# Optimization experiments

Measured on AMD Instinct MI355X. Metric: run time of the kernel, lower is better.

## Reference

```python
import math
import jax, jax.numpy as jnp
import numpy as np

B, T, C, H = 2, 4096, 512, 8  # batch, seq_len, n_embd, n_head
D = C // H                    # head_dim = 64

def setup_inputs() -> dict:
    key = jax.random.key(0)
    k1, k2, k3 = jax.random.split(key, 3)
    x = jax.random.normal(k1, (B, T, C), dtype=jnp.float32)
    # torch Linear(C, 3C, bias=False): y = x @ W.T; we store the transposed
    # weight directly so the forward is x @ W_attn.
    W_attn = jax.random.normal(k2, (C, 3 * C), dtype=jnp.float32) * 0.02
    W_proj = jax.random.normal(k3, (C, C), dtype=jnp.float32) * 0.02
    return {"x": x, "W_attn": W_attn, "W_proj": W_proj}

def reference(x, W_attn, W_proj):
    b, t, c = x.shape
    # fused QKV projection, split like .split(n_embd, dim=2)
    qkv = x @ W_attn                              # [B,T,3C]
    q, k, v = jnp.split(qkv, 3, axis=-1)          # each [B,T,C]
    def to_heads(u):
        return u.reshape(b, t, H, D).transpose(0, 2, 1, 3)  # [B,H,T,D]
    q, k, v = to_heads(q), to_heads(k), to_heads(v)
    scale = 1.0 / math.sqrt(D)
    att = jnp.einsum('bhqd,bhkd->bhqk', q, k) * scale       # [B,H,T,T]
    causal = jnp.tril(jnp.ones((t, t), dtype=bool))         # masked_fill(triu(...,1), -inf)
    att = jnp.where(causal, att, -jnp.inf)
    probs = jax.nn.softmax(att, axis=-1)
    y = jnp.einsum('bhqk,bhkd->bhqd', probs, v)             # [B,H,T,D]
    y = y.transpose(0, 2, 1, 3).reshape(b, t, c)            # [B,T,C]
    return y @ W_proj
```

## Files before the change

kernel.cpp:

```cpp
#include <hip/hip_runtime.h>
#include <hip/hip_bf16.h>
#include <stdint.h>


typedef __attribute__((ext_vector_type(8))) short short8;
typedef __attribute__((ext_vector_type(4))) float floatx4;

__device__ __forceinline__ unsigned short f2bf(float f) {
    unsigned int x = __float_as_uint(f);
    unsigned int r = x + 0x7fffu + ((x >> 16) & 1u);
    return (unsigned short)(r >> 16);
}

__device__ __forceinline__ unsigned int pk_bf16(float a, float b) {
    __hip_bfloat162 p = __float22bfloat162_rn(make_float2(a, b));
    return *reinterpret_cast<unsigned int*>(&p);
}

__global__ __launch_bounds__(256) void prep_a(
    const float* __restrict__ x, unsigned short* __restrict__ xb,
    const float* __restrict__ Wa, unsigned short* __restrict__ WaT)
{
    const int bid = blockIdx.x;
    const int tid = threadIdx.x;
    if (bid < 2048) {
        size_t i = ((size_t)bid * 256 + tid) * 8;
        float4 a = *reinterpret_cast<const float4*>(x + i);
        float4 b = *reinterpret_cast<const float4*>(x + i + 4);
        unsigned short o[8] = {f2bf(a.x), f2bf(a.y), f2bf(a.z), f2bf(a.w),
                               f2bf(b.x), f2bf(b.y), f2bf(b.z), f2bf(b.w)};
        *reinterpret_cast<uint4*>(xb + i) = *reinterpret_cast<uint4*>(o);
    } else {
        __shared__ unsigned short tile[32][34];
        const int t2 = bid - 2048;
        const int n0 = (t2 % 48) * 32, k0 = (t2 / 48) * 32;
        const int tx = tid & 31, ty = tid >> 5;
        #pragma unroll
        for (int p = 0; p < 4; ++p)
            tile[tx][ty + p * 8] = f2bf(Wa[(size_t)(k0 + ty + p * 8) * 1536 + n0 + tx]);
        __syncthreads();
        #pragma unroll
        for (int p = 0; p < 4; ++p)
            WaT[(size_t)(n0 + ty + p * 8) * 512 + k0 + tx] = tile[ty + p * 8][tx];
    }
}

__global__ __launch_bounds__(256) void transpose_wp(
    const float* __restrict__ W, unsigned short* __restrict__ Wt)
{
    __shared__ unsigned short tile[32][34];
    const int tid = threadIdx.x;
    const int tx = tid & 31, ty = tid >> 5;
    const int n0 = blockIdx.x * 32, k0 = blockIdx.y * 32;
    #pragma unroll
    for (int p = 0; p < 4; ++p)
        tile[tx][ty + p * 8] = f2bf(W[(size_t)(k0 + ty + p * 8) * 512 + n0 + tx]);
    __syncthreads();
    #pragma unroll
    for (int p = 0; p < 4; ++p)
        Wt[(size_t)(n0 + ty + p * 8) * 512 + k0 + tx] = tile[ty + p * 8][tx];
}

template<int EPI>
__global__ __launch_bounds__(256) void mm_bt(
    const unsigned short* __restrict__ A,
    const unsigned short* __restrict__ Bt,
    void* __restrict__ outp)
{
    __shared__ __align__(16) unsigned char smem[40960];

    const int tid  = threadIdx.x;
    const int wave = tid >> 6;
    const int lane = tid & 63;
    const int quad = lane >> 4;
    const int l16  = lane & 15;
    const int wr   = wave >> 1;
    const int wc   = wave & 1;
    const int m0 = blockIdx.x * 128;
    const int n0 = blockIdx.y * 128;

    floatx4 acc[4][4];
    #pragma unroll
    for (int i = 0; i < 4; ++i)
        #pragma unroll
        for (int j = 0; j < 4; ++j) acc[i][j] = (floatx4){0.f, 0.f, 0.f, 0.f};

    const int row = tid >> 1;
    const int cb  = (tid & 1) * 16;

    const unsigned short* ap = &A[(size_t)(m0 + row) * 512 + cb];
    const unsigned short* bp = &Bt[(size_t)(n0 + row) * 512 + cb];

    uint4 ra0 = *reinterpret_cast<const uint4*>(ap);
    uint4 ra1 = *reinterpret_cast<const uint4*>(ap + 8);
    uint4 rb0 = *reinterpret_cast<const uint4*>(bp);
    uint4 rb1 = *reinterpret_cast<const uint4*>(bp + 8);
    {
        auto Al = reinterpret_cast<unsigned short(*)[40]>(smem);
        auto Bl = reinterpret_cast<unsigned short(*)[40]>(smem + 10240);
        *reinterpret_cast<uint4*>(&Al[row][cb])     = ra0;
        *reinterpret_cast<uint4*>(&Al[row][cb + 8]) = ra1;
        *reinterpret_cast<uint4*>(&Bl[row][cb])     = rb0;
        *reinterpret_cast<uint4*>(&Bl[row][cb + 8]) = rb1;
    }

    for (int it = 0; it < 16; ++it) {
        __syncthreads();
        const int k0 = it * 32;
        if (it < 15) {
            ra0 = *reinterpret_cast<const uint4*>(ap + k0 + 32);
            ra1 = *reinterpret_cast<const uint4*>(ap + k0 + 40);
            rb0 = *reinterpret_cast<const uint4*>(bp + k0 + 32);
            rb1 = *reinterpret_cast<const uint4*>(bp + k0 + 40);
        }

        auto Al = reinterpret_cast<unsigned short(*)[40]>(smem + (it & 1) * 20480);
        auto Bl = reinterpret_cast<unsigned short(*)[40]>(smem + (it & 1) * 20480 + 10240);

        short8 af[4], bf[4];
        #pragma unroll
        for (int ti = 0; ti < 4; ++ti)
            af[ti] = *reinterpret_cast<const short8*>(&Al[wr * 64 + ti * 16 + l16][quad * 8]);
        #pragma unroll
        for (int tj = 0; tj < 4; ++tj)
            bf[tj] = *reinterpret_cast<const short8*>(&Bl[wc * 64 + tj * 16 + l16][quad * 8]);
        #pragma unroll
        for (int ti = 0; ti < 4; ++ti)
            #pragma unroll
            for (int tj = 0; tj < 4; ++tj)
                acc[ti][tj] = __builtin_amdgcn_mfma_f32_16x16x32_bf16(af[ti], bf[tj], acc[ti][tj], 0, 0, 0);

        if (it < 15) {
            auto An = reinterpret_cast<unsigned short(*)[40]>(smem + ((it + 1) & 1) * 20480);
            auto Bn = reinterpret_cast<unsigned short(*)[40]>(smem + ((it + 1) & 1) * 20480 + 10240);
            *reinterpret_cast<uint4*>(&An[row][cb])     = ra0;
            *reinterpret_cast<uint4*>(&An[row][cb + 8]) = ra1;
            *reinterpret_cast<uint4*>(&Bn[row][cb])     = rb0;
            *reinterpret_cast<uint4*>(&Bn[row][cb + 8]) = rb1;
        }
    }

    if (EPI == 0) {
        unsigned short* WS = (unsigned short*)outp;
        unsigned short* Qb  = WS;
        unsigned short* Kb  = WS + 4194304;
        unsigned short* Vtb = WS + 8388608;
        const int which = n0 >> 9;
        const int h = ((n0 + wc * 64) >> 6) & 7;

        if (which == 2) {
            auto Tr = reinterpret_cast<unsigned short(*)[80]>(smem);
            __syncthreads();
            #pragma unroll
            for (int ti = 0; ti < 4; ++ti)
                #pragma unroll
                for (int tj = 0; tj < 4; ++tj) {
                    unsigned int lo = pk_bf16(acc[ti][tj][0], acc[ti][tj][1]);
                    unsigned int hi = pk_bf16(acc[ti][tj][2], acc[ti][tj][3]);
                    *reinterpret_cast<uint2*>(&Tr[(wave << 6) + tj * 16 + l16][ti * 16 + quad * 4])
                        = make_uint2(lo, hi);
                }
            const int b = m0 >> 12;
            const int bh = b * 8 + h;
            const int t0g = (m0 & 4095) + wr * 64;
            const int tseg = (lane & 7) * 8;
            #pragma unroll
            for (int p = 0; p < 8; ++p) {
                int dl = p * 8 + (lane >> 3);
                uint4 v = *reinterpret_cast<const uint4*>(&Tr[(wave << 6) + dl][tseg]);
                *reinterpret_cast<uint4*>(&Vtb[((size_t)(bh * 64 + dl)) * 4096 + t0g + tseg]) = v;
            }
        } else {
            const float sc = (which == 0) ? 0.18033688f : 1.0f;
            #pragma unroll
            for (int ti = 0; ti < 4; ++ti) {
                #pragma unroll
                for (int r = 0; r < 4; ++r) {
                    int m = m0 + wr * 64 + ti * 16 + quad * 4 + r;
                    int b = m >> 12, t = m & 4095;
                    int bh = b * 8 + h;
                    #pragma unroll
                    for (int tj = 0; tj < 4; ++tj) {
                        int d = tj * 16 + l16;
                        unsigned short val = f2bf(acc[ti][tj][r] * sc);
                        if (which == 0) Qb[((size_t)bh * 4096 + t) * 64 + d] = val;
                        else            Kb[((size_t)bh * 4096 + t) * 64 + d] = val;
                    }
                }
            }
        }
    } else {
        float* Out = (float*)outp;
        #pragma unroll
        for (int ti = 0; ti < 4; ++ti) {
            #pragma unroll
            for (int r = 0; r < 4; ++r) {
                int m = m0 + wr * 64 + ti * 16 + quad * 4 + r;
                #pragma unroll
                for (int tj = 0; tj < 4; ++tj) {
                    int n = n0 + wc * 64 + tj * 16 + l16;
                    Out[(size_t)m * 512 + n] = acc[ti][tj][r];
                }
            }
        }
    }
}

__global__ __launch_bounds__(256) void attn_mfma(
    const unsigned short* __restrict__ Q,
    const unsigned short* __restrict__ K,
    const unsigned short* __restrict__ Vt,
    unsigned short* __restrict__ Y)
{
    __shared__ __align__(16) unsigned short Kc[2][64][64];
    __shared__ __align__(16) unsigned short Vc[2][64][64];
    __shared__ __align__(16) unsigned short Pc[4][32][64];

    const int tid  = threadIdx.x;
    const int wave = tid >> 6;
    const int lane = tid & 63;
    const int quad = lane >> 4;
    const int l16  = lane & 15;
    const int swz  = l16 & 7;

    const int bid = blockIdx.x;
    const int bh  = bid & 15;
    const int j   = (bid >> 4) & 15;
    const int g   = bid >> 8;
    const int qb  = (g == 0) ? j : (31 - j);
    const int m0  = qb * 128;

    const unsigned short* Qp = Q  + (size_t)bh * (4096 * 64);
    const unsigned short* Kp = K  + (size_t)bh * (4096 * 64);
    const unsigned short* Vp = Vt + (size_t)bh * (64 * 4096);

    short8 qf[2][2];
    #pragma unroll
    for (int qt = 0; qt < 2; ++qt) {
        const size_t qr = (size_t)(m0 + wave * 32 + qt * 16 + l16) * 64;
        qf[qt][0] = *reinterpret_cast<const short8*>(&Qp[qr + quad * 8]);
        qf[qt][1] = *reinterpret_cast<const short8*>(&Qp[qr + 32 + quad * 8]);
    }

    short8 ones;
    #pragma unroll
    for (int i = 0; i < 8; ++i) ones[i] = (short)0x3F80;

    floatx4 o[2][4];
    #pragma unroll
    for (int qt = 0; qt < 2; ++qt)
        #pragma unroll
        for (int n = 0; n < 4; ++n) o[qt][n] = (floatx4){0.f, 0.f, 0.f, 0.f};
    floatx4 o4[2] = {{0, 0, 0, 0}, {0, 0, 0, 0}};

    const int r0 = tid >> 3;
    const int r1 = r0 + 32;
    const int cc = tid & 7;
    const int c0 = cc * 8;
    const int sc = ((cc ^ (r0 & 7)) << 3);

    uint4 rk0 = *reinterpret_cast<const uint4*>(&Kp[(size_t)r0 * 64 + c0]);
    uint4 rk1 = *reinterpret_cast<const uint4*>(&Kp[(size_t)r1 * 64 + c0]);
    uint4 rv0 = *reinterpret_cast<const uint4*>(&Vp[(size_t)r0 * 4096 + c0]);
    uint4 rv1 = *reinterpret_cast<const uint4*>(&Vp[(size_t)r1 * 4096 + c0]);
    *reinterpret_cast<uint4*>(&Kc[0][r0][sc]) = rk0;
    *reinterpret_cast<uint4*>(&Kc[0][r1][sc]) = rk1;
    *reinterpret_cast<uint4*>(&Vc[0][r0][sc]) = rv0;
    *reinterpret_cast<uint4*>(&Vc[0][r1][sc]) = rv1;

    const int nt   = 2 * qb + 2;
    const int diag = 2 * qb + (wave >> 1);

    for (int kt = 0; kt < nt; ++kt) {
        __syncthreads();
        const int cur = kt & 1;
        const int nxt = cur ^ 1;

        if (kt + 1 < nt) {
            const int jn = (kt + 1) * 64;
            rk0 = *reinterpret_cast<const uint4*>(&Kp[(size_t)(jn + r0) * 64 + c0]);
            rk1 = *reinterpret_cast<const uint4*>(&Kp[(size_t)(jn + r1) * 64 + c0]);
            rv0 = *reinterpret_cast<const uint4*>(&Vp[(size_t)r0 * 4096 + jn + c0]);
            rv1 = *reinterpret_cast<const uint4*>(&Vp[(size_t)r1 * 4096 + jn + c0]);
        }

        if (kt <= diag) {
            const bool dg = (kt == diag);
            #pragma unroll
            for (int ct = 0; ct < 4; ++ct) {
                const unsigned short* kr = &Kc[cur][ct * 16 + l16][0];
                short8 a0 = *reinterpret_cast<const short8*>(kr + ((quad ^ swz) << 3));
                short8 a1 = *reinterpret_cast<const short8*>(kr + (((4 + quad) ^ swz) << 3));
                #pragma unroll
                for (int qt = 0; qt < 2; ++qt) {
                    floatx4 s = {0, 0, 0, 0};
                    s = __builtin_amdgcn_mfma_f32_16x16x32_bf16(a0, qf[qt][0], s, 0, 0, 0);
                    s = __builtin_amdgcn_mfma_f32_16x16x32_bf16(a1, qf[qt][1], s, 0, 0, 0);
                    float sv[4];
                    #pragma unroll
                    for (int r = 0; r < 4; ++r) sv[r] = s[r];
                    if (dg) {
                        const int ql = (wave & 1) * 32 + qt * 16 + l16;
                        #pragma unroll
                        for (int r = 0; r < 4; ++r) {
                            int keyl = ct * 16 + quad * 4 + r;
                            sv[r] = (keyl <= ql) ? sv[r] : -1e30f;
                        }
                    }
                    #pragma unroll
                    for (int r = 0; r < 4; ++r) sv[r] = __builtin_amdgcn_exp2f(sv[r]);
                    unsigned int d0 = pk_bf16(sv[0], sv[1]);
                    unsigned int d1 = pk_bf16(sv[2], sv[3]);
                    *reinterpret_cast<uint2*>(
                        &Pc[wave][qt * 16 + l16]
                           [(((ct * 2 + (quad >> 1)) ^ swz) << 3) + (quad & 1) * 4])
                        = make_uint2(d0, d1);
                }
            }

            short8 pa[2][2];
            #pragma unroll
            for (int qt = 0; qt < 2; ++qt) {
                const unsigned short* pr = &Pc[wave][qt * 16 + l16][0];
                pa[qt][0] = *reinterpret_cast<const short8*>(pr + ((quad ^ swz) << 3));
                pa[qt][1] = *reinterpret_cast<const short8*>(pr + (((4 + quad) ^ swz) << 3));
            }
            #pragma unroll
            for (int qt = 0; qt < 2; ++qt) {
                o4[qt] = __builtin_amdgcn_mfma_f32_16x16x32_bf16(pa[qt][0], ones, o4[qt], 0, 0, 0);
                o4[qt] = __builtin_amdgcn_mfma_f32_16x16x32_bf16(pa[qt][1], ones, o4[qt], 0, 0, 0);
            }
            #pragma unroll
            for (int n = 0; n < 4; ++n) {
                const unsigned short* vr = &Vc[cur][n * 16 + l16][0];
                short8 b0 = *reinterpret_cast<const short8*>(vr + ((quad ^ swz) << 3));
                short8 b1 = *reinterpret_cast<const short8*>(vr + (((4 + quad) ^ swz) << 3));
                #pragma unroll
                for (int qt = 0; qt < 2; ++qt) {
                    o[qt][n] = __builtin_amdgcn_mfma_f32_16x16x32_bf16(pa[qt][0], b0, o[qt][n], 0, 0, 0);
                    o[qt][n] = __builtin_amdgcn_mfma_f32_16x16x32_bf16(pa[qt][1], b1, o[qt][n], 0, 0, 0);
                }
            }
        }

        if (kt + 1 < nt) {
            *reinterpret_cast<uint4*>(&Kc[nxt][r0][sc]) = rk0;
            *reinterpret_cast<uint4*>(&Kc[nxt][r1][sc]) = rk1;
            *reinterpret_cast<uint4*>(&Vc[nxt][r0][sc]) = rv0;
            *reinterpret_cast<uint4*>(&Vc[nxt][r1][sc]) = rv1;
        }
    }

    const int b = bh >> 3, h = bh & 7;
    #pragma unroll
    for (int qt = 0; qt < 2; ++qt)
        #pragma unroll
        for (int r = 0; r < 4; ++r) {
            float inv = 1.0f / o4[qt][r];
            int t = m0 + wave * 32 + qt * 16 + quad * 4 + r;
            #pragma unroll
            for (int n = 0; n < 4; ++n)
                Y[((size_t)(b * 4096 + t)) * 512 + h * 64 + n * 16 + l16] = f2bf(o[qt][n][r] * inv);
        }
}

extern "C" void kernel_launch(void* const* d_in, const int* in_sizes, int n_in,
                              void* d_out, int out_size, void* d_ws, size_t ws_size,
                              hipStream_t stream) {
    const float* x  = (const float*)d_in[0];
    const float* Wa = (const float*)d_in[1];
    const float* Wp = (const float*)d_in[2];
    float* out = (float*)d_out;
    unsigned short* ws = (unsigned short*)d_ws;

    unsigned short* Qb  = ws;
    unsigned short* Kb  = ws + 4194304;
    unsigned short* Vtb = ws + 8388608;
    unsigned short* Yb  = ws + 12582912;
    unsigned short* WaT = Yb;
    unsigned short* WpT = Qb;
    unsigned short* xb  = (unsigned short*)d_out;

    prep_a<<<dim3(2816), dim3(256), 0, stream>>>(x, xb, Wa, WaT);
    mm_bt<0><<<dim3(64, 12), dim3(256), 0, stream>>>(xb, WaT, (void*)ws);
    attn_mfma<<<dim3(512), dim3(256), 0, stream>>>(Qb, Kb, Vtb, Yb);
    transpose_wp<<<dim3(16, 16), dim3(256), 0, stream>>>(Wp, WpT);
    mm_bt<1><<<dim3(64, 4), dim3(256), 0, stream>>>(Yb, WpT, (void*)out);
}
```

Measured before the change: 176.9 us.

## Shrink attention blocks to 64 query rows with 2 waves and 1024 blocks

The attention kernel now uses 128-thread blocks that each cover 64 query rows, so the launch has 1024 blocks instead of 512. The per-wave diagonal skip goes away, since both waves share the same key-tile range. The query-block ordering is remapped to pair short and long causal rows for load balance. The aim is finer-grained parallelism, less idle time for waves past the diagonal, and smaller LDS per block for higher occupancy. In exchange, each K/V tile loaded into LDS is reused by half as many query rows, which doubles K/V traffic.

```diff
diff --git a/kernel.cpp b/kernel.cpp
--- a/kernel.cpp
+++ b/kernel.cpp
@@ -206,7 +206,7 @@
     }
 }
 
-__global__ __launch_bounds__(256) void attn_mfma(
+__global__ __launch_bounds__(128) void attn_mfma(
     const unsigned short* __restrict__ Q,
     const unsigned short* __restrict__ K,
     const unsigned short* __restrict__ Vt,
@@ -214,7 +214,7 @@
 {
     __shared__ __align__(16) unsigned short Kc[2][64][64];
     __shared__ __align__(16) unsigned short Vc[2][64][64];
-    __shared__ __align__(16) unsigned short Pc[4][32][64];
+    __shared__ __align__(16) unsigned short Pc[2][32][64];
 
     const int tid  = threadIdx.x;
     const int wave = tid >> 6;
@@ -227,8 +227,8 @@
     const int bh  = bid & 15;
     const int j   = (bid >> 4) & 15;
     const int g   = bid >> 8;
-    const int qb  = (g == 0) ? j : (31 - j);
-    const int m0  = qb * 128;
+    const int qb  = (g == 0) ? j : (g == 1) ? (63 - j) : (g == 2) ? (16 + j) : (47 - j);
+    const int m0  = qb * 64;
 
     const unsigned short* Qp = Q  + (size_t)bh * (4096 * 64);
     const unsigned short* Kp = K  + (size_t)bh * (4096 * 64);
@@ -253,23 +253,24 @@
         for (int n = 0; n < 4; ++n) o[qt][n] = (floatx4){0.f, 0.f, 0.f, 0.f};
     floatx4 o4[2] = {{0, 0, 0, 0}, {0, 0, 0, 0}};
 
-    const int r0 = tid >> 3;
-    const int r1 = r0 + 32;
-    const int cc = tid & 7;
-    const int c0 = cc * 8;
-    const int sc = ((cc ^ (r0 & 7)) << 3);
-
-    uint4 rk0 = *reinterpret_cast<const uint4*>(&Kp[(size_t)r0 * 64 + c0]);
-    uint4 rk1 = *reinterpret_cast<const uint4*>(&Kp[(size_t)r1 * 64 + c0]);
-    uint4 rv0 = *reinterpret_cast<const uint4*>(&Vp[(size_t)r0 * 4096 + c0]);
-    uint4 rv1 = *reinterpret_cast<const uint4*>(&Vp[(size_t)r1 * 4096 + c0]);
-    *reinterpret_cast<uint4*>(&Kc[0][r0][sc]) = rk0;
-    *reinterpret_cast<uint4*>(&Kc[0][r1][sc]) = rk1;
-    *reinterpret_cast<uint4*>(&Vc[0][r0][sc]) = rv0;
-    *reinterpret_cast<uint4*>(&Vc[0][r1][sc]) = rv1;
-
-    const int nt   = 2 * qb + 2;
-    const int diag = 2 * qb + (wave >> 1);
+    const int ch  = tid & 7;
+    const int rr  = tid >> 3;
+    const int c0  = ch * 8;
+    const int scs = ((ch ^ (rr & 7)) << 3);
+
+    uint4 rk[4], rv[4];
+    #pragma unroll
+    for (int i = 0; i < 4; ++i) {
+        rk[i] = *reinterpret_cast<const uint4*>(&Kp[(size_t)(rr + 16 * i) * 64 + c0]);
+        rv[i] = *reinterpret_cast<const uint4*>(&Vp[(size_t)(rr + 16 * i) * 4096 + c0]);
+    }
+    #pragma unroll
+    for (int i = 0; i < 4; ++i) {
+        *reinterpret_cast<uint4*>(&Kc[0][rr + 16 * i][scs]) = rk[i];
+        *reinterpret_cast<uint4*>(&Vc[0][rr + 16 * i][scs]) = rv[i];
+    }
+
+    const int nt = qb + 1;
 
     for (int kt = 0; kt < nt; ++kt) {
         __syncthreads();
@@ -278,76 +279,76 @@
 
         if (kt + 1 < nt) {
             const int jn = (kt + 1) * 64;
-            rk0 = *reinterpret_cast<const uint4*>(&Kp[(size_t)(jn + r0) * 64 + c0]);
-            rk1 = *reinterpret_cast<const uint4*>(&Kp[(size_t)(jn + r1) * 64 + c0]);
-            rv0 = *reinterpret_cast<const uint4*>(&Vp[(size_t)r0 * 4096 + jn + c0]);
-            rv1 = *reinterpret_cast<const uint4*>(&Vp[(size_t)r1 * 4096 + jn + c0]);
-        }
-
-        if (kt <= diag) {
-            const bool dg = (kt == diag);
-            #pragma unroll
-            for (int ct = 0; ct < 4; ++ct) {
-                const unsigned short* kr = &Kc[cur][ct * 16 + l16][0];
-                short8 a0 = *reinterpret_cast<const short8*>(kr + ((quad ^ swz) << 3));
-                short8 a1 = *reinterpret_cast<const short8*>(kr + (((4 + quad) ^ swz) << 3));
-                #pragma unroll
-                for (int qt = 0; qt < 2; ++qt) {
-                    floatx4 s = {0, 0, 0, 0};
-                    s = __builtin_amdgcn_mfma_f32_16x16x32_bf16(a0, qf[qt][0], s, 0, 0, 0);
-                    s = __builtin_amdgcn_mfma_f32_16x16x32_bf16(a1, qf[qt][1], s, 0, 0, 0);
-                    float sv[4];
+            #pragma unroll
+            for (int i = 0; i < 4; ++i) {
+                rk[i] = *reinterpret_cast<const uint4*>(&Kp[(size_t)(jn + rr + 16 * i) * 64 + c0]);
+                rv[i] = *reinterpret_cast<const uint4*>(&Vp[(size_t)(rr + 16 * i) * 4096 + jn + c0]);
+            }
+        }
+
+        const bool dg = (kt == qb);
+        #pragma unroll
+        for (int ct = 0; ct < 4; ++ct) {
+            const unsigned short* kr = &Kc[cur][ct * 16 + l16][0];
+            short8 a0 = *reinterpret_cast<const short8*>(kr + ((quad ^ swz) << 3));
+            short8 a1 = *reinterpret_cast<const short8*>(kr + (((4 + quad) ^ swz) << 3));
+            #pragma unroll
+            for (int qt = 0; qt < 2; ++qt) {
+                floatx4 s = {0, 0, 0, 0};
+                s = __builtin_amdgcn_mfma_f32_16x16x32_bf16(a0, qf[qt][0], s, 0, 0, 0);
+                s = __builtin_amdgcn_mfma_f32_16x16x32_bf16(a1, qf[qt][1], s, 0, 0, 0);
+                float sv[4];
+                #pragma unroll
+                for (int r = 0; r < 4; ++r) sv[r] = s[r];
+                if (dg) {
+                    const int ql = wave * 32 + qt * 16 + l16;
                     #pragma unroll
-                    for (int r = 0; r < 4; ++r) sv[r] = s[r];
-                    if (dg) {
-                        const int ql = (wave & 1) * 32 + qt * 16 + l16;
-                        #pragma unroll
-                        for (int r = 0; r < 4; ++r) {
-                            int keyl = ct * 16 + quad * 4 + r;
-                            sv[r] = (keyl <= ql) ? sv[r] : -1e30f;
-                        }
+                    for (int r = 0; r < 4; ++r) {
+                        int keyl = ct * 16 + quad * 4 + r;
+                        sv[r] = (keyl <= ql) ? sv[r] : -1e30f;
                     }
-                    #pragma unroll
-                    for (int r = 0; r < 4; ++r) sv[r] = __builtin_amdgcn_exp2f(sv[r]);
-                    unsigned int d0 = pk_bf16(sv[0], sv[1]);
-                    unsigned int d1 = pk_bf16(sv[2], sv[3]);
-                    *reinterpret_cast<uint2*>(
-                        &Pc[wave][qt * 16 + l16]
-                           [(((ct * 2 + (quad >> 1)) ^ swz) << 3) + (quad & 1) * 4])
-                        = make_uint2(d0, d1);
                 }
-            }
-
-            short8 pa[2][2];
+                #pragma unroll
+                for (int r = 0; r < 4; ++r) sv[r] = __builtin_amdgcn_exp2f(sv[r]);
+                unsigned int d0 = pk_bf16(sv[0], sv[1]);
+                unsigned int d1 = pk_bf16(sv[2], sv[3]);
+                *reinterpret_cast<uint2*>(
+                    &Pc[wave][qt * 16 + l16]
+                       [(((ct * 2 + (quad >> 1)) ^ swz) << 3) + (quad & 1) * 4])
+                    = make_uint2(d0, d1);
+            }
+        }
+
+        short8 pa[2][2];
+        #pragma unroll
+        for (int qt = 0; qt < 2; ++qt) {
+            const unsigned short* pr = &Pc[wave][qt * 16 + l16][0];
+            pa[qt][0] = *reinterpret_cast<const short8*>(pr + ((quad ^ swz) << 3));
+            pa[qt][1] = *reinterpret_cast<const short8*>(pr + (((4 + quad) ^ swz) << 3));
+        }
+        #pragma unroll
+        for (int qt = 0; qt < 2; ++qt) {
+            o4[qt] = __builtin_amdgcn_mfma_f32_16x16x32_bf16(pa[qt][0], ones, o4[qt], 0, 0, 0);
+            o4[qt] = __builtin_amdgcn_mfma_f32_16x16x32_bf16(pa[qt][1], ones, o4[qt], 0, 0, 0);
+        }
+        #pragma unroll
+        for (int n = 0; n < 4; ++n) {
+            const unsigned short* vr = &Vc[cur][n * 16 + l16][0];
+            short8 b0 = *reinterpret_cast<const short8*>(vr + ((quad ^ swz) << 3));
+            short8 b1 = *reinterpret_cast<const short8*>(vr + (((4 + quad) ^ swz) << 3));
             #pragma unroll
             for (int qt = 0; qt < 2; ++qt) {
-                const unsigned short* pr = &Pc[wave][qt * 16 + l16][0];
-                pa[qt][0] = *reinterpret_cast<const short8*>(pr + ((quad ^ swz) << 3));
-                pa[qt][1] = *reinterpret_cast<const short8*>(pr + (((4 + quad) ^ swz) << 3));
-            }
-            #pragma unroll
-            for (int qt = 0; qt < 2; ++qt) {
-                o4[qt] = __builtin_amdgcn_mfma_f32_16x16x32_bf16(pa[qt][0], ones, o4[qt], 0, 0, 0);
-                o4[qt] = __builtin_amdgcn_mfma_f32_16x16x32_bf16(pa[qt][1], ones, o4[qt], 0, 0, 0);
-            }
-            #pragma unroll
-            for (int n = 0; n < 4; ++n) {
-                const unsigned short* vr = &Vc[cur][n * 16 + l16][0];
-                short8 b0 = *reinterpret_cast<const short8*>(vr + ((quad ^ swz) << 3));
-                short8 b1 = *reinterpret_cast<const short8*>(vr + (((4 + quad) ^ swz) << 3));
-                #pragma unroll
-                for (int qt = 0; qt < 2; ++qt) {
-                    o[qt][n] = __builtin_amdgcn_mfma_f32_16x16x32_bf16(pa[qt][0], b0, o[qt][n], 0, 0, 0);
-                    o[qt][n] = __builtin_amdgcn_mfma_f32_16x16x32_bf16(pa[qt][1], b1, o[qt][n], 0, 0, 0);
-                }
+                o[qt][n] = __builtin_amdgcn_mfma_f32_16x16x32_bf16(pa[qt][0], b0, o[qt][n], 0, 0, 0);
+                o[qt][n] = __builtin_amdgcn_mfma_f32_16x16x32_bf16(pa[qt][1], b1, o[qt][n], 0, 0, 0);
             }
         }
 
         if (kt + 1 < nt) {
-            *reinterpret_cast<uint4*>(&Kc[nxt][r0][sc]) = rk0;
-            *reinterpret_cast<uint4*>(&Kc[nxt][r1][sc]) = rk1;
-            *reinterpret_cast<uint4*>(&Vc[nxt][r0][sc]) = rv0;
-            *reinterpret_cast<uint4*>(&Vc[nxt][r1][sc]) = rv1;
+            #pragma unroll
+            for (int i = 0; i < 4; ++i) {
+                *reinterpret_cast<uint4*>(&Kc[nxt][rr + 16 * i][scs]) = rk[i];
+                *reinterpret_cast<uint4*>(&Vc[nxt][rr + 16 * i][scs]) = rv[i];
+            }
         }
     }
 
@@ -383,7 +384,7 @@
 
     prep_a<<<dim3(2816), dim3(256), 0, stream>>>(x, xb, Wa, WaT);
     mm_bt<0><<<dim3(64, 12), dim3(256), 0, stream>>>(xb, WaT, (void*)ws);
-    attn_mfma<<<dim3(512), dim3(256), 0, stream>>>(Qb, Kb, Vtb, Yb);
+    attn_mfma<<<dim3(1024), dim3(128), 0, stream>>>(Qb, Kb, Vtb, Yb);
     transpose_wp<<<dim3(16, 16), dim3(256), 0, stream>>>(Wp, WpT);
     mm_bt<1><<<dim3(64, 4), dim3(256), 0, stream>>>(Yb, WpT, (void*)out);
 }
```

Result: slower. 186.3 us (+5.3%).

## Halve attention query tile to 64 rows and double grid size

Applied to the files above, without the earlier changes.

The attention kernel now assigns 64 query rows per block (16 per wave) instead of 128, launching 1024 blocks with a four-way balanced causal ordering. This is meant to improve occupancy and load balance and to drop the idle-wave diagonal handling, since every wave now processes the same key tiles. The cost is that K/V tiles are loaded and read from LDS for half as many queries, doubling K/V global and LDS traffic per unit of work.

```diff
diff --git a/kernel.cpp b/kernel.cpp
--- a/kernel.cpp
+++ b/kernel.cpp
@@ -214,7 +214,7 @@
 {
     __shared__ __align__(16) unsigned short Kc[2][64][64];
     __shared__ __align__(16) unsigned short Vc[2][64][64];
-    __shared__ __align__(16) unsigned short Pc[4][32][64];
+    __shared__ __align__(16) unsigned short Pc[4][16][64];
 
     const int tid  = threadIdx.x;
     const int wave = tid >> 6;
@@ -224,34 +224,27 @@
     const int swz  = l16 & 7;
 
     const int bid = blockIdx.x;
-    const int bh  = bid & 15;
-    const int j   = (bid >> 4) & 15;
-    const int g   = bid >> 8;
-    const int qb  = (g == 0) ? j : (31 - j);
-    const int m0  = qb * 128;
+    const int bh = bid & 15;
+    const int j  = (bid >> 4) & 15;
+    const int g  = bid >> 8;
+    const int qb = (g == 0) ? j : (g == 1) ? (63 - j) : (g == 2) ? (16 + j) : (47 - j);
+    const int m0 = qb * 64;
 
     const unsigned short* Qp = Q  + (size_t)bh * (4096 * 64);
     const unsigned short* Kp = K  + (size_t)bh * (4096 * 64);
     const unsigned short* Vp = Vt + (size_t)bh * (64 * 4096);
 
-    short8 qf[2][2];
-    #pragma unroll
-    for (int qt = 0; qt < 2; ++qt) {
-        const size_t qr = (size_t)(m0 + wave * 32 + qt * 16 + l16) * 64;
-        qf[qt][0] = *reinterpret_cast<const short8*>(&Qp[qr + quad * 8]);
-        qf[qt][1] = *reinterpret_cast<const short8*>(&Qp[qr + 32 + quad * 8]);
-    }
+    const int qrow = m0 + wave * 16 + l16;
+    short8 qf[2];
+    qf[0] = *reinterpret_cast<const short8*>(&Qp[(size_t)qrow * 64 + quad * 8]);
+    qf[1] = *reinterpret_cast<const short8*>(&Qp[(size_t)qrow * 64 + 32 + quad * 8]);
 
     short8 ones;
     #pragma unroll
     for (int i = 0; i < 8; ++i) ones[i] = (short)0x3F80;
 
-    floatx4 o[2][4];
-    #pragma unroll
-    for (int qt = 0; qt < 2; ++qt)
-        #pragma unroll
-        for (int n = 0; n < 4; ++n) o[qt][n] = (floatx4){0.f, 0.f, 0.f, 0.f};
-    floatx4 o4[2] = {{0, 0, 0, 0}, {0, 0, 0, 0}};
+    floatx4 o[4] = {{0,0,0,0},{0,0,0,0},{0,0,0,0},{0,0,0,0}};
+    floatx4 o4 = {0, 0, 0, 0};
 
     const int r0 = tid >> 3;
     const int r1 = r0 + 32;
@@ -268,15 +261,12 @@
     *reinterpret_cast<uint4*>(&Vc[0][r0][sc]) = rv0;
     *reinterpret_cast<uint4*>(&Vc[0][r1][sc]) = rv1;
 
-    const int nt   = 2 * qb + 2;
-    const int diag = 2 * qb + (wave >> 1);
-
-    for (int kt = 0; kt < nt; ++kt) {
+    for (int kt = 0; kt <= qb; ++kt) {
         __syncthreads();
         const int cur = kt & 1;
         const int nxt = cur ^ 1;
 
-        if (kt + 1 < nt) {
+        if (kt < qb) {
             const int jn = (kt + 1) * 64;
             rk0 = *reinterpret_cast<const uint4*>(&Kp[(size_t)(jn + r0) * 64 + c0]);
             rk1 = *reinterpret_cast<const uint4*>(&Kp[(size_t)(jn + r1) * 64 + c0]);
@@ -284,66 +274,54 @@
             rv1 = *reinterpret_cast<const uint4*>(&Vp[(size_t)r1 * 4096 + jn + c0]);
         }
 
-        if (kt <= diag) {
-            const bool dg = (kt == diag);
-            #pragma unroll
-            for (int ct = 0; ct < 4; ++ct) {
-                const unsigned short* kr = &Kc[cur][ct * 16 + l16][0];
-                short8 a0 = *reinterpret_cast<const short8*>(kr + ((quad ^ swz) << 3));
-                short8 a1 = *reinterpret_cast<const short8*>(kr + (((4 + quad) ^ swz) << 3));
+        const bool dg = (kt == qb);
+        #pragma unroll
+        for (int ct = 0; ct < 4; ++ct) {
+            const unsigned short* kr = &Kc[cur][ct * 16 + l16][0];
+            short8 a0 = *reinterpret_cast<const short8*>(kr + ((quad ^ swz) << 3));
+            short8 a1 = *reinterpret_cast<const short8*>(kr + (((4 + quad) ^ swz) << 3));
+            floatx4 s = {0, 0, 0, 0};
+            s = __builtin_amdgcn_mfma_f32_16x16x32_bf16(a0, qf[0], s, 0, 0, 0);
+            s = __builtin_amdgcn_mfma_f32_16x16x32_bf16(a1, qf[1], s, 0, 0, 0);
+            float sv[4];
+            #pragma unroll
+            for (int r = 0; r < 4; ++r) sv[r] = s[r];
+            if (dg) {
+                const int ql = wave * 16 + l16;
                 #pragma unroll
-                for (int qt = 0; qt < 2; ++qt) {
-                    floatx4 s = {0, 0, 0, 0};
-                    s = __builtin_amdgcn_mfma_f32_16x16x32_bf16(a0, qf[qt][0], s, 0, 0, 0);
-                    s = __builtin_amdgcn_mfma_f32_16x16x32_bf16(a1, qf[qt][1], s, 0, 0, 0);
-                    float sv[4];
-                    #pragma unroll
-                    for (int r = 0; r < 4; ++r) sv[r] = s[r];
-                    if (dg) {
-                        const int ql = (wave & 1) * 32 + qt * 16 + l16;
-                        #pragma unroll
-                        for (int r = 0; r < 4; ++r) {
-                            int keyl = ct * 16 + quad * 4 + r;
-                            sv[r] = (keyl <= ql) ? sv[r] : -1e30f;
-                        }
-                    }
-                    #pragma unroll
-                    for (int r = 0; r < 4; ++r) sv[r] = __builtin_amdgcn_exp2f(sv[r]);
-                    unsigned int d0 = pk_bf16(sv[0], sv[1]);
-                    unsigned int d1 = pk_bf16(sv[2], sv[3]);
-                    *reinterpret_cast<uint2*>(
-                        &Pc[wave][qt * 16 + l16]
-                           [(((ct * 2 + (quad >> 1)) ^ swz) << 3) + (quad & 1) * 4])
-                        = make_uint2(d0, d1);
+                for (int r = 0; r < 4; ++r) {
+                    int keyl = ct * 16 + quad * 4 + r;
+                    sv[r] = (keyl <= ql) ? sv[r] : -1e30f;
                 }
             }
-
-            short8 pa[2][2];
-            #pragma unroll
-            for (int qt = 0; qt < 2; ++qt) {
-                const unsigned short* pr = &Pc[wave][qt * 16 + l16][0];
-                pa[qt][0] = *reinterpret_cast<const short8*>(pr + ((quad ^ swz) << 3));
-                pa[qt][1] = *reinterpret_cast<const short8*>(pr + (((4 + quad) ^ swz) << 3));
-            }
-            #pragma unroll
-            for (int qt = 0; qt < 2; ++qt) {
-                o4[qt] = __builtin_amdgcn_mfma_f32_16x16x32_bf16(pa[qt][0], ones, o4[qt], 0, 0, 0);
-                o4[qt] = __builtin_amdgcn_mfma_f32_16x16x32_bf16(pa[qt][1], ones, o4[qt], 0, 0, 0);
-            }
-            #pragma unroll
-            for (int n = 0; n < 4; ++n) {
-                const unsigned short* vr = &Vc[cur][n * 16 + l16][0];
-                short8 b0 = *reinterpret_cast<const short8*>(vr + ((quad ^ swz) << 3));
-                short8 b1 = *reinterpret_cast<const short8*>(vr + (((4 + quad) ^ swz) << 3));
-                #pragma unroll
-                for (int qt = 0; qt < 2; ++qt) {
-                    o[qt][n] = __builtin_amdgcn_mfma_f32_16x16x32_bf16(pa[qt][0], b0, o[qt][n], 0, 0, 0);
-                    o[qt][n] = __builtin_amdgcn_mfma_f32_16x16x32_bf16(pa[qt][1], b1, o[qt][n], 0, 0, 0);
-                }
-            }
-        }
-
-        if (kt + 1 < nt) {
+            #pragma unroll
+            for (int r = 0; r < 4; ++r) sv[r] = __builtin_amdgcn_exp2f(sv[r]);
+            unsigned int d0 = pk_bf16(sv[0], sv[1]);
+            unsigned int d1 = pk_bf16(sv[2], sv[3]);
+            *reinterpret_cast<uint2*>(
+                &Pc[wave][l16][(((ct * 2 + (quad >> 1)) ^ swz) << 3) + (quad & 1) * 4])
+                = make_uint2(d0, d1);
+        }
+
+        short8 pa[2];
+        {
+            const unsigned short* pr = &Pc[wave][l16][0];
+            pa[0] = *reinterpret_cast<const short8*>(pr + ((quad ^ swz) << 3));
+            pa[1] = *reinterpret_cast<const short8*>(pr + (((4 + quad) ^ swz) << 3));
+        }
+        #pragma unroll
+        for (int kk = 0; kk < 2; ++kk)
+            o4 = __builtin_amdgcn_mfma_f32_16x16x32_bf16(pa[kk], ones, o4, 0, 0, 0);
+        #pragma unroll
+        for (int n = 0; n < 4; ++n) {
+            const unsigned short* vr = &Vc[cur][n * 16 + l16][0];
+            short8 b0 = *reinterpret_cast<const short8*>(vr + ((quad ^ swz) << 3));
+            short8 b1 = *reinterpret_cast<const short8*>(vr + (((4 + quad) ^ swz) << 3));
+            o[n] = __builtin_amdgcn_mfma_f32_16x16x32_bf16(pa[0], b0, o[n], 0, 0, 0);
+            o[n] = __builtin_amdgcn_mfma_f32_16x16x32_bf16(pa[1], b1, o[n], 0, 0, 0);
+        }
+
+        if (kt < qb) {
             *reinterpret_cast<uint4*>(&Kc[nxt][r0][sc]) = rk0;
             *reinterpret_cast<uint4*>(&Kc[nxt][r1][sc]) = rk1;
             *reinterpret_cast<uint4*>(&Vc[nxt][r0][sc]) = rv0;
@@ -353,15 +331,13 @@
 
     const int b = bh >> 3, h = bh & 7;
     #pragma unroll
-    for (int qt = 0; qt < 2; ++qt)
-        #pragma unroll
-        for (int r = 0; r < 4; ++r) {
-            float inv = 1.0f / o4[qt][r];
-            int t = m0 + wave * 32 + qt * 16 + quad * 4 + r;
-            #pragma unroll
-            for (int n = 0; n < 4; ++n)
-                Y[((size_t)(b * 4096 + t)) * 512 + h * 64 + n * 16 + l16] = f2bf(o[qt][n][r] * inv);
-        }
+    for (int r = 0; r < 4; ++r) {
+        float inv = 1.0f / o4[r];
+        int t = m0 + wave * 16 + quad * 4 + r;
+        #pragma unroll
+        for (int n = 0; n < 4; ++n)
+            Y[((size_t)(b * 4096 + t)) * 512 + h * 64 + n * 16 + l16] = f2bf(o[n][r] * inv);
+    }
 }
 
 extern "C" void kernel_launch(void* const* d_in, const int* in_sizes, int n_in,
@@ -383,7 +359,7 @@
 
     prep_a<<<dim3(2816), dim3(256), 0, stream>>>(x, xb, Wa, WaT);
     mm_bt<0><<<dim3(64, 12), dim3(256), 0, stream>>>(xb, WaT, (void*)ws);
-    attn_mfma<<<dim3(512), dim3(256), 0, stream>>>(Qb, Kb, Vtb, Yb);
+    attn_mfma<<<dim3(1024), dim3(256), 0, stream>>>(Qb, Kb, Vtb, Yb);
     transpose_wp<<<dim3(16, 16), dim3(256), 0, stream>>>(Wp, WpT);
     mm_bt<1><<<dim3(64, 4), dim3(256), 0, stream>>>(Yb, WpT, (void*)out);
 }
```

Measured after the change: 165.2 us. 1.07x faster.
